# Kernel optimization log

Hardware: AMD Instinct MI355X
Metric: run time of the kernel (lower is better)

Reference implementation:

```python
import jax, jax.numpy as jnp
import numpy as np

NTIPS = 128   # taxa
NSITES = 1024 # unique site patterns
BS = 32       # batch of trees


def _make_pairs(ntips, bs, seed=0):
    """Valid postorder child/parent triples for random caterpillar trees.

    Mirrors Parsimony._score's child_parent_pairs: [ntips-1, bs, 3], where the
    last step's torch parent=-1 is rewritten to the last state slot 2*ntips-2.
    """
    rng = np.random.default_rng(seed)
    N = 2 * ntips - 1
    pairs = np.zeros((ntips - 1, bs, 3), dtype=np.int32)
    for b in range(bs):
        leaves = rng.permutation(ntips)
        pairs[0, b] = [leaves[0], leaves[1], ntips]
        for i in range(1, ntips - 3):
            pairs[i, b] = [ntips + i - 1, leaves[i + 1], ntips + i]
        root = 2 * ntips - 3
        pairs[ntips - 3, b] = [2 * ntips - 4, leaves[ntips - 2], root]
        pairs[ntips - 2, b] = [root, leaves[ntips - 1], N - 1]
    return pairs


def setup_inputs() -> dict:
    key = jax.random.key(0)
    k1, k2 = jax.random.split(key)
    # one-hot nucleotide states over 5 symbols (A,G,C,T,-)
    nuc = jax.random.randint(k1, (NTIPS, NSITES), 0, 4)
    L = jax.nn.one_hot(nuc, 5, dtype=jnp.int32).transpose(0, 2, 1)  # [ntips,5,S]
    site_counts = jax.random.randint(k2, (NSITES,), 1, 100).astype(jnp.int32)
    pairs = jnp.asarray(_make_pairs(NTIPS, BS))  # [ntips-1, bs, 3]
    return {"L": L, "site_counts": site_counts, "pairs": pairs}


def reference(L, site_counts, pairs):
    ntips, _, S = L.shape
    steps, bs, _ = pairs.shape
    N = 2 * ntips - 1
    base = jnp.concatenate(
        [L, jnp.zeros((N - ntips, 5, S), dtype=L.dtype)], axis=0)  # [N,5,S]
    state0 = jnp.tile(base[None], (bs, 1, 1, 1))   # [bs,N,5,S]
    score0 = jnp.zeros((bs, S), jnp.int32)
    barange = jnp.arange(bs)

    def step(carry, pair):
        state, score = carry
        child, parent = pair[:, :2], pair[:, 2]            # [bs,2], [bs]
        cs = state[barange[:, None], child]                # gather -> [bs,2,5,S]
        inter = cs[:, 0] * cs[:, 1]                        # [bs,5,S]
        union = ((cs[:, 0] + cs[:, 1]) > 0).astype(L.dtype)
        empty = inter.sum(axis=1, keepdims=True) == 0      # [bs,1,S]
        nxt = jnp.where(empty, union, inter)               # Fitch rule
        state = state.at[barange, parent].set(nxt)         # scatter
        score = score + empty[:, 0].astype(jnp.int32)
        return (state, score), None

    (_, score), _ = jax.lax.scan(step, (state0, score0), pairs)
    return jnp.sum(score * site_counts[None, :], axis=-1)  # [bs]
```

## Files before the change

kernel.cpp:

```cpp
#include <hip/hip_runtime.h>
#include <stdint.h>

#define NTIPS 128
#define NSITES 1024
#define BS 32
#define STEPS 127
#define SB 64

__global__ __launch_bounds__(256) void pack_leaves(const int* __restrict__ L,
                                                   uint8_t* __restrict__ packed) {
    int i = blockIdx.x * 256 + threadIdx.x;
    int tip = i >> 10, site = i & 1023;
    const int* b = L + tip * 5 * NSITES + site;
    int m = b[0] | (b[NSITES] << 1) | (b[2 * NSITES] << 2) |
            (b[3 * NSITES] << 3) | (b[4 * NSITES] << 4);
    packed[i] = (uint8_t)m;
}

__global__ __launch_bounds__(64) void fitch_kernel(const int* __restrict__ L,
                                                   const int* __restrict__ site_counts,
                                                   const int* __restrict__ pairs,
                                                   const uint8_t* __restrict__ packed,
                                                   int use_packed,
                                                   int* __restrict__ out) {
    __shared__ int     leafm[NTIPS][SB];
    __shared__ uint8_t internal[STEPS][SB];
    __shared__ int     spairs[STEPS * 3];

    const int tid      = threadIdx.x;
    const int batch    = blockIdx.x >> 4;
    const int siteBase = (blockIdx.x & 15) * SB;
    const int site     = siteBase + tid;

    for (int i = tid; i < STEPS * 3; i += 64) {
        int s = i / 3, j = i - s * 3;
        spairs[i] = pairs[s * (BS * 3) + batch * 3 + j];
    }

    if (use_packed) {
        for (int i = tid; i < NTIPS * (SB / 4); i += 64) {
            int tip = i >> 4, j = i & 15;
            unsigned d = ((const unsigned*)(packed + (tip << 10) + siteBase))[j];
            int4 v = make_int4(d & 255, (d >> 8) & 255, (d >> 16) & 255, (d >> 24) & 255);
            *(int4*)&leafm[tip][j * 4] = v;
        }
    } else {
        for (int tip = 0; tip < NTIPS; ++tip) {
            const int* b = L + tip * 5 * NSITES + site;
            leafm[tip][tid] = b[0] | (b[NSITES] << 1) | (b[2 * NSITES] << 2) |
                              (b[3 * NSITES] << 3) | (b[4 * NSITES] << 4);
        }
    }
    __syncthreads();

    int lastP = -1;
    int lastV = 0;
    int score = 0;
    for (int s = 0; s < STEPS; ++s) {
        int c0 = __builtin_amdgcn_readfirstlane(spairs[3 * s]);
        int c1 = __builtin_amdgcn_readfirstlane(spairs[3 * s + 1]);
        int p  = __builtin_amdgcn_readfirstlane(spairs[3 * s + 2]);
        int m0, m1;
        if (c0 == lastP)     m0 = lastV;
        else if (c0 < NTIPS) m0 = leafm[c0][tid];
        else                 m0 = (int)internal[c0 - NTIPS][tid];
        if (c1 == lastP)     m1 = lastV;
        else if (c1 < NTIPS) m1 = leafm[c1][tid];
        else                 m1 = (int)internal[c1 - NTIPS][tid];
        int inter = m0 & m1;
        int nxt   = inter ? inter : (m0 | m1);
        score    += (inter == 0);
        internal[p - NTIPS][tid] = (uint8_t)nxt;
        lastP = p;
        lastV = nxt;
    }

    int val = score * site_counts[site];
    #pragma unroll
    for (int off = 32; off; off >>= 1) val += __shfl_down(val, off);
    if (tid == 0) atomicAdd(&out[batch], val);
}

extern "C" void kernel_launch(void* const* d_in, const int* in_sizes, int n_in,
                              void* d_out, int out_size, void* d_ws, size_t ws_size,
                              hipStream_t stream) {
    const int* L           = (const int*)d_in[0];
    const int* site_counts = (const int*)d_in[1];
    const int* pairs       = (const int*)d_in[2];
    int* out               = (int*)d_out;

    hipMemsetAsync(out, 0, BS * sizeof(int), stream);

    const size_t packed_bytes = (size_t)NTIPS * NSITES;
    int use_packed = (ws_size >= packed_bytes) ? 1 : 0;
    uint8_t* packed = (uint8_t*)d_ws;

    if (use_packed) {
        pack_leaves<<<dim3((NTIPS * NSITES) / 256), dim3(256), 0, stream>>>(L, packed);
    }
    fitch_kernel<<<dim3(BS * (NSITES / SB)), dim3(64), 0, stream>>>(
        L, site_counts, pairs, packed, use_packed, out);
}
```

Baseline: 86.53 us.

## Unify leaf and internal state in byte LDS, read pairs directly, fold memset

Merges leaf masks and internal node states into one byte-per-site shared array, shrinking shared memory and removing the leaf/internal branch. Pairs are now read from global memory through uniform loads inside an unrolled loop instead of being staged in shared memory. Zeroing the output moves into the pack kernel, which drops a separate memset launch. In exchange, the serial step loop now carries global-load latency, which unrolling is meant to hide.

```diff
diff --git a/kernel.cpp b/kernel.cpp
--- a/kernel.cpp
+++ b/kernel.cpp
@@ -5,11 +5,14 @@
 #define NSITES 1024
 #define BS 32
 #define STEPS 127
+#define NNODES 255
 #define SB 64
 
 __global__ __launch_bounds__(256) void pack_leaves(const int* __restrict__ L,
-                                                   uint8_t* __restrict__ packed) {
+                                                   uint8_t* __restrict__ packed,
+                                                   int* __restrict__ out) {
     int i = blockIdx.x * 256 + threadIdx.x;
+    if (blockIdx.x == 0 && threadIdx.x < BS) out[threadIdx.x] = 0;
     int tip = i >> 10, site = i & 1023;
     const int* b = L + tip * 5 * NSITES + site;
     int m = b[0] | (b[NSITES] << 1) | (b[2 * NSITES] << 2) |
@@ -23,54 +26,50 @@
                                                    const uint8_t* __restrict__ packed,
                                                    int use_packed,
                                                    int* __restrict__ out) {
-    __shared__ int     leafm[NTIPS][SB];
-    __shared__ uint8_t internal[STEPS][SB];
-    __shared__ int     spairs[STEPS * 3];
+    __shared__ uint8_t state[NNODES][SB];
 
     const int tid      = threadIdx.x;
     const int batch    = blockIdx.x >> 4;
     const int siteBase = (blockIdx.x & 15) * SB;
     const int site     = siteBase + tid;
 
-    for (int i = tid; i < STEPS * 3; i += 64) {
-        int s = i / 3, j = i - s * 3;
-        spairs[i] = pairs[s * (BS * 3) + batch * 3 + j];
-    }
-
     if (use_packed) {
-        for (int i = tid; i < NTIPS * (SB / 4); i += 64) {
-            int tip = i >> 4, j = i & 15;
-            unsigned d = ((const unsigned*)(packed + (tip << 10) + siteBase))[j];
-            int4 v = make_int4(d & 255, (d >> 8) & 255, (d >> 16) & 255, (d >> 24) & 255);
-            *(int4*)&leafm[tip][j * 4] = v;
+        #pragma unroll 8
+        for (int k = 0; k < 32; ++k) {
+            int i = (k << 6) + tid;
+            int t = i >> 4, j = i & 15;
+            uint32_t d = *(const uint32_t*)(packed + (t << 10) + siteBase + (j << 2));
+            ((uint32_t*)state)[i] = d;
         }
     } else {
-        for (int tip = 0; tip < NTIPS; ++tip) {
-            const int* b = L + tip * 5 * NSITES + site;
-            leafm[tip][tid] = b[0] | (b[NSITES] << 1) | (b[2 * NSITES] << 2) |
-                              (b[3 * NSITES] << 3) | (b[4 * NSITES] << 4);
+        const int* Lp = L + site;
+        #pragma unroll 8
+        for (int t = 0; t < NTIPS; ++t) {
+            const int* b = Lp + t * 5 * NSITES;
+            int m = b[0] | (b[NSITES] << 1) | (b[2 * NSITES] << 2) |
+                    (b[3 * NSITES] << 3) | (b[4 * NSITES] << 4);
+            state[t][tid] = (uint8_t)m;
         }
     }
     __syncthreads();
 
+    const int* pb = pairs + batch * 3;
     int lastP = -1;
     int lastV = 0;
     int score = 0;
+    #pragma unroll 8
     for (int s = 0; s < STEPS; ++s) {
-        int c0 = __builtin_amdgcn_readfirstlane(spairs[3 * s]);
-        int c1 = __builtin_amdgcn_readfirstlane(spairs[3 * s + 1]);
-        int p  = __builtin_amdgcn_readfirstlane(spairs[3 * s + 2]);
-        int m0, m1;
-        if (c0 == lastP)     m0 = lastV;
-        else if (c0 < NTIPS) m0 = leafm[c0][tid];
-        else                 m0 = (int)internal[c0 - NTIPS][tid];
-        if (c1 == lastP)     m1 = lastV;
-        else if (c1 < NTIPS) m1 = leafm[c1][tid];
-        else                 m1 = (int)internal[c1 - NTIPS][tid];
+        const int c0 = pb[s * (BS * 3)];
+        const int c1 = pb[s * (BS * 3) + 1];
+        const int p  = pb[s * (BS * 3) + 2];
+        int r0 = (int)state[c0][tid];
+        int r1 = (int)state[c1][tid];
+        int m0 = (c0 == lastP) ? lastV : r0;
+        int m1 = (c1 == lastP) ? lastV : r1;
         int inter = m0 & m1;
         int nxt   = inter ? inter : (m0 | m1);
         score    += (inter == 0);
-        internal[p - NTIPS][tid] = (uint8_t)nxt;
+        state[p][tid] = (uint8_t)nxt;
         lastP = p;
         lastV = nxt;
     }
@@ -89,14 +88,14 @@
     const int* pairs       = (const int*)d_in[2];
     int* out               = (int*)d_out;
 
-    hipMemsetAsync(out, 0, BS * sizeof(int), stream);
-
     const size_t packed_bytes = (size_t)NTIPS * NSITES;
     int use_packed = (ws_size >= packed_bytes) ? 1 : 0;
     uint8_t* packed = (uint8_t*)d_ws;
 
     if (use_packed) {
-        pack_leaves<<<dim3((NTIPS * NSITES) / 256), dim3(256), 0, stream>>>(L, packed);
+        pack_leaves<<<dim3((NTIPS * NSITES) / 256), dim3(256), 0, stream>>>(L, packed, out);
+    } else {
+        hipMemsetAsync(out, 0, BS * sizeof(int), stream);
     }
     fitch_kernel<<<dim3(BS * (NSITES / SB)), dim3(64), 0, stream>>>(
         L, site_counts, pairs, packed, use_packed, out);
```

Result: no change. 88.16 us (+1.9%).
